# Kernel tuning notes

Hardware: AMD Instinct MI355X
Metric: run time of the kernel (lower is better)

Reference implementation:

```python
import jax, jax.numpy as jnp
import numpy as np

N_USERS = 50000
N_ENTITIES = 100000
D = 64
R = 16
E_UI = 1500000
E_KG = 100000


def setup_inputs() -> dict:
    key = jax.random.key(0)
    ks = jax.random.split(key, 7)
    s = 1.0 / np.sqrt(D)  # ~xavier scale
    return {
        "user_indices": jnp.arange(N_USERS, dtype=jnp.int32),
        "item_indices": jnp.arange(N_ENTITIES, dtype=jnp.int32),
        "edge_index_ui": jax.random.randint(ks[0], (2, E_UI), 0, N_USERS + N_ENTITIES, dtype=jnp.int32),
        "edge_index_kg": jax.random.randint(ks[1], (2, E_KG), 0, N_ENTITIES, dtype=jnp.int32),
        "edge_type_kg": jax.random.randint(ks[2], (E_KG,), 0, R, dtype=jnp.int32),
        "user_table": (jax.random.normal(ks[3], (N_USERS, D)) * s).astype(jnp.float32),
        "entity_table": (jax.random.normal(ks[4], (N_ENTITIES, D)) * s).astype(jnp.float32),
        "W": (jax.random.normal(ks[5], (D, D)) * s).astype(jnp.float32),
        "W_r": (jax.random.normal(ks[6], (R, D, D)) * s).astype(jnp.float32),
    }


def _kgat_layer(x, edge_index, W, W_r, edge_type=None):
    # PyG aggr='add', flow source_to_target: x_j = x[src], x_i = x[dst], scatter to dst
    src, dst = edge_index[0], edge_index[1]
    x_j = x[src]  # [E, D]
    x_i = x[dst]  # [E, D]
    if edge_type is None:
        x_j_t = x_j @ W  # [E, D]
    else:
        # per-edge relation-specific transform: bmm(x_j[:,None,:], W_r[edge_type])
        x_j_t = jnp.einsum('ed,edo->eo', x_j, W_r[edge_type])
    # bi-interaction attention
    x_i_t = x_i @ W
    logits = jnp.sum(x_i_t * x_j_t, axis=1, keepdims=True)  # [E, 1]
    logits = jax.nn.leaky_relu(logits, negative_slope=0.2)
    scores = jax.nn.softmax(logits, axis=0)  # GLOBAL softmax over all edges (as in source)
    msg = scores * x_j_t  # [E, D]
    return jax.ops.segment_sum(msg, dst, num_segments=x.shape[0])


def reference(user_indices, item_indices, edge_index_ui, edge_index_kg, edge_type_kg,
              user_table, entity_table, W, W_r):
    user_embeds = user_table[user_indices]      # [n_users, D]
    item_embeds = entity_table[item_indices]    # [n_entities, D]
    x = jnp.concatenate([user_embeds, item_embeds], axis=0)
    # single layer (layer_dims = [embed_dim])
    x_ui = _kgat_layer(x, edge_index_ui, W, W_r, edge_type=None)
    x_kg = _kgat_layer(item_embeds, edge_index_kg, W, W_r, edge_type=edge_type_kg)
    x = x.at[N_USERS:].add(x_kg)  # faithful to source: overwritten by next line (dead store)
    x = jax.nn.relu(x_ui)
    # F.dropout(training=False) -> identity in eval mode
    return (x[:N_USERS], x[N_USERS:])
```

## Files before the change

kernel.cpp:

```cpp
#include <hip/hip_runtime.h>

#define NU 50000
#define NE 100000
#define NN 150000
#define DD 64
#define EUI 1500000

#define TPB 256
#define NBLK 2048
#define NXB 2344
#define NXH (NXB + NBLK)
#define NBF2 9375
#define NSC 9375

#define XWB_OFF    0ull
#define CNT_OFF    4800000ull
#define SCAL_OFF   4950000ull
#define PSUM_OFF   4950004ull
#define XWQ_OFF    4959424ull

__device__ __forceinline__ unsigned bfpack(float a, float b) {
  unsigned ua = __float_as_uint(a);
  ua = (ua + 0x7fffu + ((ua >> 16) & 1u)) >> 16;
  unsigned ub = __float_as_uint(b);
  ub = (ub + 0x7fffu + ((ub >> 16) & 1u)) & 0xffff0000u;
  return (ua & 0xffffu) | ub;
}

__device__ __forceinline__ unsigned q7pack4(float a, float b, float c, float d) {
  const float m = fmaxf(fmaxf(fabsf(a), fabsf(b)), fmaxf(fabsf(c), fabsf(d)));
  int E = -20;
  if (m >= 3.0517578125e-05f) {
    E = (int)((__float_as_uint(m) >> 23) & 0xffu) - 132;
    E = max(-20, min(-5, E));
  }
  const float s = __uint_as_float((unsigned)(127 - E) << 23);
  const int qa = max(-64, min(63, (int)rintf(a * s)));
  const int qb = max(-64, min(63, (int)rintf(b * s)));
  const int qc = max(-64, min(63, (int)rintf(c * s)));
  const int qd = max(-64, min(63, (int)rintf(d * s)));
  return ((unsigned)(E + 20) << 28) |
         (unsigned)(qa & 0x7f) | ((unsigned)(qb & 0x7f) << 7) |
         ((unsigned)(qc & 0x7f) << 14) | ((unsigned)(qd & 0x7f) << 21);
}

__device__ __forceinline__ void q7unpack4(unsigned v, float& s, float& a,
                                          float& b, float& c, float& d) {
  s = __uint_as_float(((v >> 28) + 107u) << 23);
  a = (float)((int)(v << 25) >> 25);
  b = (float)((int)(v << 18) >> 25);
  c = (float)((int)(v << 11) >> 25);
  d = (float)((int)(v << 4) >> 25);
}

template <int CTRL>
__device__ __forceinline__ float dpp_add(float x) {
  int y = __builtin_amdgcn_update_dpp(0, __float_as_int(x), CTRL, 0xF, 0xF, false);
  return x + __int_as_float(y);
}
__device__ __forceinline__ float row16_sum(float x) {
  x = dpp_add<0x124>(x);
  x = dpp_add<0x128>(x);
  x = dpp_add<0xB1>(x);
  x = dpp_add<0x4E>(x);
  return x;
}

__global__ __launch_bounds__(TPB) void k_xw_hist(const int* __restrict__ uidx,
                                                 const int* __restrict__ iidx,
                                                 const float* __restrict__ ut,
                                                 const float* __restrict__ et,
                                                 const float* __restrict__ W,
                                                 unsigned* __restrict__ xwb,
                                                 unsigned* __restrict__ xwq,
                                                 const int* __restrict__ ei,
                                                 unsigned* __restrict__ cnt,
                                                 int* __restrict__ ssrcp) {
  const int bi = blockIdx.x;
  int idx;
  bool hist;
  if (bi < 2 * NBLK) { hist = (bi & 1); idx = bi >> 1; }
  else               { hist = false;    idx = bi - NBLK; }

  if (hist) {
    for (int e = idx * TPB + threadIdx.x; e < EUI; e += NBLK * TPB) {
      const int dst = ei[EUI + e];
      const int src = ei[e];
      const unsigned r = atomicAdd(&cnt[dst], 1u);
      if (r < 64u) ssrcp[((size_t)dst << 6) + r] = src;
    }
    return;
  }

  __shared__ float Ws[DD * DD];
  __shared__ float Xs[64 * 68];
  const int t = threadIdx.x;
  {
    const float4* W4 = (const float4*)W;
    float4* Ws4 = (float4*)Ws;
#pragma unroll
    for (int i = 0; i < 4; ++i) Ws4[t + i * TPB] = W4[t + i * TPB];
  }
  {
    const int rl = t >> 2, ch = t & 3;
    int row = idx * 64 + rl;
    if (row >= NN) row = NN - 1;
    const float4* s4 = (const float4*)((row < NU)
        ? ut + (size_t)uidx[row] * DD
        : et + (size_t)iidx[row - NU] * DD);
    float4* x4 = (float4*)(Xs + rl * 68);
#pragma unroll
    for (int j = 0; j < 4; ++j) x4[ch + 4 * j] = s4[ch + 4 * j];
  }
  __syncthreads();
  const int q = t & 15, g = t >> 4;
  float4 acc[4] = {{0,0,0,0},{0,0,0,0},{0,0,0,0},{0,0,0,0}};
  const float* __restrict__ wsq = Ws + 4 * q;
  const float* __restrict__ xsg = Xs + (4 * g) * 68;
#pragma unroll 1
  for (int kc = 0; kc < 16; ++kc) {
    const float4 w0 = *(const float4*)(wsq + (4 * kc + 0) * DD);
    const float4 w1 = *(const float4*)(wsq + (4 * kc + 1) * DD);
    const float4 w2 = *(const float4*)(wsq + (4 * kc + 2) * DD);
    const float4 w3 = *(const float4*)(wsq + (4 * kc + 3) * DD);
#pragma unroll
    for (int i = 0; i < 4; ++i) {
      const float4 x = *(const float4*)(xsg + i * 68 + 4 * kc);
      acc[i].x = fmaf(x.x, w0.x, acc[i].x);
      acc[i].y = fmaf(x.x, w0.y, acc[i].y);
      acc[i].z = fmaf(x.x, w0.z, acc[i].z);
      acc[i].w = fmaf(x.x, w0.w, acc[i].w);
      acc[i].x = fmaf(x.y, w1.x, acc[i].x);
      acc[i].y = fmaf(x.y, w1.y, acc[i].y);
      acc[i].z = fmaf(x.y, w1.z, acc[i].z);
      acc[i].w = fmaf(x.y, w1.w, acc[i].w);
      acc[i].x = fmaf(x.z, w2.x, acc[i].x);
      acc[i].y = fmaf(x.z, w2.y, acc[i].y);
      acc[i].z = fmaf(x.z, w2.z, acc[i].z);
      acc[i].w = fmaf(x.z, w2.w, acc[i].w);
      acc[i].x = fmaf(x.w, w3.x, acc[i].x);
      acc[i].y = fmaf(x.w, w3.y, acc[i].y);
      acc[i].z = fmaf(x.w, w3.z, acc[i].z);
      acc[i].w = fmaf(x.w, w3.w, acc[i].w);
    }
  }
#pragma unroll
  for (int i = 0; i < 4; ++i) {
    const int row = idx * 64 + 4 * g + i;
    if (row < NN) {
      uint2 p;
      p.x = bfpack(acc[i].x, acc[i].y);
      p.y = bfpack(acc[i].z, acc[i].w);
      ((uint2*)(xwb + (size_t)row * 32))[q] = p;
      xwq[(size_t)row * 16 + q] = q7pack4(acc[i].x, acc[i].y, acc[i].z, acc[i].w);
    }
  }
}

__global__ __launch_bounds__(TPB) void k_fused(const unsigned* __restrict__ cnt,
                                               const int* ssrcp,
                                               const unsigned* __restrict__ xwb,
                                               const unsigned* __restrict__ xwq,
                                               float* out,
                                               float* __restrict__ psum) {
  const int lane = threadIdx.x & 63;
  const int wv = threadIdx.x >> 6;
  const int sub = lane >> 4;
  const int q = lane & 15;
  const int n = blockIdx.x * 16 + wv * 4 + sub;
  const uint2* __restrict__ x2 = (const uint2*)xwb;
  const uint2 dv = x2[(size_t)n * 16 + q];
  const float vd0 = __uint_as_float(dv.x << 16);
  const float vd1 = __uint_as_float(dv.x & 0xffff0000u);
  const float vd2 = __uint_as_float(dv.y << 16);
  const float vd3 = __uint_as_float(dv.y & 0xffff0000u);
  const int deg = min((int)cnt[n], 64);
  int dmax = deg;
  dmax = max(dmax, __shfl_xor(dmax, 16, 64));
  dmax = max(dmax, __shfl_xor(dmax, 32, 64));
  const size_t base = (size_t)n << 6;
  const int nit = (dmax + 3) >> 2;
  float a0 = 0.f, a1 = 0.f, a2 = 0.f, a3 = 0.f, wacc = 0.f;
  int sl0 = ssrcp[base], sl1 = ssrcp[base + 1];
  int sl2 = ssrcp[base + 2], sl3 = ssrcp[base + 3];
  for (int ii = 0; ii < nit; ++ii) {
    const int it = 4 * ii;
    int s0 = sl0, s1 = sl1, s2 = sl2, s3 = sl3;
    if (ii + 1 < nit) {
      sl0 = ssrcp[base + it + 4];
      sl1 = ssrcp[base + it + 5];
      sl2 = ssrcp[base + it + 6];
      sl3 = ssrcp[base + it + 7];
    }
    const bool act0 = it < deg;
    const bool act1 = it + 1 < deg;
    const bool act2 = it + 2 < deg;
    const bool act3 = it + 3 < deg;
    if (!act0) s0 = 0;
    if (!act1) s1 = 0;
    if (!act2) s2 = 0;
    if (!act3) s3 = 0;
    const unsigned sv0 = xwq[(size_t)s0 * 16 + q];
    const unsigned sv1 = xwq[(size_t)s1 * 16 + q];
    const unsigned sv2 = xwq[(size_t)s2 * 16 + q];
    const unsigned sv3 = xwq[(size_t)s3 * 16 + q];
    float se0, u0, u1, u2, u3;
    float se1, t0, t1, t2, t3;
    float se2, g0, g1, g2, g3;
    float se3, h0, h1, h2, h3;
    q7unpack4(sv0, se0, u0, u1, u2, u3);
    q7unpack4(sv1, se1, t0, t1, t2, t3);
    q7unpack4(sv2, se2, g0, g1, g2, g3);
    q7unpack4(sv3, se3, h0, h1, h2, h3);
    float p0 = vd0 * u0;
    p0 = fmaf(vd1, u1, p0); p0 = fmaf(vd2, u2, p0); p0 = fmaf(vd3, u3, p0);
    float p1 = vd0 * t0;
    p1 = fmaf(vd1, t1, p1); p1 = fmaf(vd2, t2, p1); p1 = fmaf(vd3, t3, p1);
    float p2 = vd0 * g0;
    p2 = fmaf(vd1, g1, p2); p2 = fmaf(vd2, g2, p2); p2 = fmaf(vd3, g3, p2);
    float p3 = vd0 * h0;
    p3 = fmaf(vd1, h1, p3); p3 = fmaf(vd2, h2, p3); p3 = fmaf(vd3, h3, p3);
    p0 *= se0;
    p1 *= se1;
    p2 *= se2;
    p3 *= se3;
    p0 = row16_sum(p0);
    p1 = row16_sum(p1);
    p2 = row16_sum(p2);
    p3 = row16_sum(p3);
    const float l0 = (p0 > 0.f) ? p0 : 0.2f * p0;
    const float l1 = (p1 > 0.f) ? p1 : 0.2f * p1;
    const float l2 = (p2 > 0.f) ? p2 : 0.2f * p2;
    const float l3 = (p3 > 0.f) ? p3 : 0.2f * p3;
    float w0 = __expf(l0);
    float w1 = __expf(l1);
    float w2 = __expf(l2);
    float w3 = __expf(l3);
    if (!act0) w0 = 0.f;
    if (!act1) w1 = 0.f;
    if (!act2) w2 = 0.f;
    if (!act3) w3 = 0.f;
    const float ws0 = w0 * se0;
    const float ws1 = w1 * se1;
    const float ws2 = w2 * se2;
    const float ws3 = w3 * se3;
    a0 = fmaf(ws0, u0, a0); a1 = fmaf(ws0, u1, a1);
    a2 = fmaf(ws0, u2, a2); a3 = fmaf(ws0, u3, a3);
    a0 = fmaf(ws1, t0, a0); a1 = fmaf(ws1, t1, a1);
    a2 = fmaf(ws1, t2, a2); a3 = fmaf(ws1, t3, a3);
    a0 = fmaf(ws2, g0, a0); a1 = fmaf(ws2, g1, a1);
    a2 = fmaf(ws2, g2, a2); a3 = fmaf(ws2, g3, a3);
    a0 = fmaf(ws3, h0, a0); a1 = fmaf(ws3, h1, a1);
    a2 = fmaf(ws3, h2, a2); a3 = fmaf(ws3, h3, a3);
    wacc += (w0 + w1) + (w2 + w3);
  }
  float4 r = {a0, a1, a2, a3};
  ((float4*)(out + (size_t)n * DD))[q] = r;
  __shared__ float sm[16];
  if (q == 0) sm[wv * 4 + sub] = wacc;
  __syncthreads();
  if (threadIdx.x == 0) {
    float s = 0.f;
#pragma unroll
    for (int i = 0; i < 16; ++i) s += sm[i];
    psum[blockIdx.x] = s;
  }
}

__global__ __launch_bounds__(TPB) void k_rsum(const float* __restrict__ psum,
                                              float* __restrict__ scal) {
  float s = 0.f;
  for (int i = threadIdx.x; i < NBF2; i += TPB) s += psum[i];
#pragma unroll
  for (int off = 32; off; off >>= 1) s += __shfl_xor(s, off, 64);
  __shared__ float sm[4];
  if ((threadIdx.x & 63) == 0) sm[threadIdx.x >> 6] = s;
  __syncthreads();
  if (threadIdx.x == 0) scal[0] = sm[0] + sm[1] + sm[2] + sm[3];
}

__global__ __launch_bounds__(TPB) void k_scale(float* __restrict__ out,
                                               const float* __restrict__ scal) {
  const float inv = 1.0f / scal[0];
  const int i = blockIdx.x * TPB + threadIdx.x;
  float4* o4 = (float4*)out;
  float4 v = o4[i];
  v.x = fmaxf(v.x * inv, 0.f);
  v.y = fmaxf(v.y * inv, 0.f);
  v.z = fmaxf(v.z * inv, 0.f);
  v.w = fmaxf(v.w * inv, 0.f);
  o4[i] = v;
}

extern "C" void kernel_launch(void* const* d_in, const int* in_sizes, int n_in,
                              void* d_out, int out_size, void* d_ws, size_t ws_size,
                              hipStream_t stream) {
  const int* uidx = (const int*)d_in[0];
  const int* iidx = (const int*)d_in[1];
  const int* ei_ui = (const int*)d_in[2];
  const float* ut = (const float*)d_in[5];
  const float* et = (const float*)d_in[6];
  const float* W = (const float*)d_in[7];

  float* out = (float*)d_out;
  float* ws = (float*)d_ws;
  unsigned* xwb = (unsigned*)(ws + XWB_OFF);
  unsigned* cnt = (unsigned*)(ws + CNT_OFF);
  float* scal = ws + SCAL_OFF;
  float* psum = ws + PSUM_OFF;
  unsigned* xwq = (unsigned*)(ws + XWQ_OFF);
  int* ssrcp = (int*)d_out;

  (void)hipMemsetAsync(cnt, 0, (size_t)NN * sizeof(unsigned), stream);

  k_xw_hist<<<NXH, TPB, 0, stream>>>(uidx, iidx, ut, et, W, xwb, xwq, ei_ui,
                                     cnt, ssrcp);
  k_fused<<<NBF2, TPB, 0, stream>>>(cnt, ssrcp, xwb, xwq, out, psum);
  k_rsum<<<1, TPB, 0, stream>>>(psum, scal);
  k_scale<<<NSC, TPB, 0, stream>>>(out, scal);
}
```

Measured before the change: 263.1 us.

## Split histogram by destination range to overlap second half with gather of first

The edge histogram/bucketing is split into two destination ranges. The first half runs alongside the XW transform, and the second half runs in the same launch as the aggregation of the first half of nodes. The remaining nodes are aggregated in a third kernel. This aims to hide the atomic bucketing cost behind compute, but each histogram pass now reads the full edge list twice, adding extra dst reads and divergent skips. The neighbor-index prefetch also becomes a single int4 load.

```diff
diff --git a/kernel.cpp b/kernel.cpp
--- a/kernel.cpp
+++ b/kernel.cpp
@@ -5,11 +5,15 @@
 #define NN 150000
 #define DD 64
 #define EUI 1500000
+#define SPLIT 75008
 
 #define TPB 256
 #define NBLK 2048
 #define NXB 2344
 #define NXH (NXB + NBLK)
+#define NBFA 4688
+#define NBFB 4687
+#define NHF (NBFA + NBLK)
 #define NBF2 9375
 #define NSC 9375
 
@@ -66,108 +70,31 @@
   return x;
 }
 
-__global__ __launch_bounds__(TPB) void k_xw_hist(const int* __restrict__ uidx,
-                                                 const int* __restrict__ iidx,
-                                                 const float* __restrict__ ut,
-                                                 const float* __restrict__ et,
-                                                 const float* __restrict__ W,
-                                                 unsigned* __restrict__ xwb,
-                                                 unsigned* __restrict__ xwq,
-                                                 const int* __restrict__ ei,
-                                                 unsigned* __restrict__ cnt,
-                                                 int* __restrict__ ssrcp) {
-  const int bi = blockIdx.x;
-  int idx;
-  bool hist;
-  if (bi < 2 * NBLK) { hist = (bi & 1); idx = bi >> 1; }
-  else               { hist = false;    idx = bi - NBLK; }
-
-  if (hist) {
-    for (int e = idx * TPB + threadIdx.x; e < EUI; e += NBLK * TPB) {
-      const int dst = ei[EUI + e];
-      const int src = ei[e];
-      const unsigned r = atomicAdd(&cnt[dst], 1u);
-      if (r < 64u) ssrcp[((size_t)dst << 6) + r] = src;
-    }
-    return;
-  }
-
-  __shared__ float Ws[DD * DD];
-  __shared__ float Xs[64 * 68];
-  const int t = threadIdx.x;
-  {
-    const float4* W4 = (const float4*)W;
-    float4* Ws4 = (float4*)Ws;
-#pragma unroll
-    for (int i = 0; i < 4; ++i) Ws4[t + i * TPB] = W4[t + i * TPB];
-  }
-  {
-    const int rl = t >> 2, ch = t & 3;
-    int row = idx * 64 + rl;
-    if (row >= NN) row = NN - 1;
-    const float4* s4 = (const float4*)((row < NU)
-        ? ut + (size_t)uidx[row] * DD
-        : et + (size_t)iidx[row - NU] * DD);
-    float4* x4 = (float4*)(Xs + rl * 68);
-#pragma unroll
-    for (int j = 0; j < 4; ++j) x4[ch + 4 * j] = s4[ch + 4 * j];
-  }
-  __syncthreads();
-  const int q = t & 15, g = t >> 4;
-  float4 acc[4] = {{0,0,0,0},{0,0,0,0},{0,0,0,0},{0,0,0,0}};
-  const float* __restrict__ wsq = Ws + 4 * q;
-  const float* __restrict__ xsg = Xs + (4 * g) * 68;
-#pragma unroll 1
-  for (int kc = 0; kc < 16; ++kc) {
-    const float4 w0 = *(const float4*)(wsq + (4 * kc + 0) * DD);
-    const float4 w1 = *(const float4*)(wsq + (4 * kc + 1) * DD);
-    const float4 w2 = *(const float4*)(wsq + (4 * kc + 2) * DD);
-    const float4 w3 = *(const float4*)(wsq + (4 * kc + 3) * DD);
-#pragma unroll
-    for (int i = 0; i < 4; ++i) {
-      const float4 x = *(const float4*)(xsg + i * 68 + 4 * kc);
-      acc[i].x = fmaf(x.x, w0.x, acc[i].x);
-      acc[i].y = fmaf(x.x, w0.y, acc[i].y);
-      acc[i].z = fmaf(x.x, w0.z, acc[i].z);
-      acc[i].w = fmaf(x.x, w0.w, acc[i].w);
-      acc[i].x = fmaf(x.y, w1.x, acc[i].x);
-      acc[i].y = fmaf(x.y, w1.y, acc[i].y);
-      acc[i].z = fmaf(x.y, w1.z, acc[i].z);
-      acc[i].w = fmaf(x.y, w1.w, acc[i].w);
-      acc[i].x = fmaf(x.z, w2.x, acc[i].x);
-      acc[i].y = fmaf(x.z, w2.y, acc[i].y);
-      acc[i].z = fmaf(x.z, w2.z, acc[i].z);
-      acc[i].w = fmaf(x.z, w2.w, acc[i].w);
-      acc[i].x = fmaf(x.w, w3.x, acc[i].x);
-      acc[i].y = fmaf(x.w, w3.y, acc[i].y);
-      acc[i].z = fmaf(x.w, w3.z, acc[i].z);
-      acc[i].w = fmaf(x.w, w3.w, acc[i].w);
-    }
-  }
-#pragma unroll
-  for (int i = 0; i < 4; ++i) {
-    const int row = idx * 64 + 4 * g + i;
-    if (row < NN) {
-      uint2 p;
-      p.x = bfpack(acc[i].x, acc[i].y);
-      p.y = bfpack(acc[i].z, acc[i].w);
-      ((uint2*)(xwb + (size_t)row * 32))[q] = p;
-      xwq[(size_t)row * 16 + q] = q7pack4(acc[i].x, acc[i].y, acc[i].z, acc[i].w);
-    }
-  }
-}
-
-__global__ __launch_bounds__(TPB) void k_fused(const unsigned* __restrict__ cnt,
-                                               const int* ssrcp,
-                                               const unsigned* __restrict__ xwb,
-                                               const unsigned* __restrict__ xwq,
-                                               float* out,
-                                               float* __restrict__ psum) {
+__device__ __forceinline__ void hist_body(int idx, const int* __restrict__ ei,
+                                          unsigned* __restrict__ cnt,
+                                          int* __restrict__ ssrcp,
+                                          int lo, int hi) {
+  for (int e = idx * TPB + threadIdx.x; e < EUI; e += NBLK * TPB) {
+    const int dst = ei[EUI + e];
+    if (dst < lo || dst >= hi) continue;
+    const int src = ei[e];
+    const unsigned r = atomicAdd(&cnt[dst], 1u);
+    if (r < 64u) ssrcp[((size_t)dst << 6) + r] = src;
+  }
+}
+
+__device__ __forceinline__ void fused_tile(int tile,
+                                           const unsigned* __restrict__ cnt,
+                                           const int* ssrcp,
+                                           const unsigned* __restrict__ xwb,
+                                           const unsigned* __restrict__ xwq,
+                                           float* out,
+                                           float* __restrict__ psum) {
   const int lane = threadIdx.x & 63;
   const int wv = threadIdx.x >> 6;
   const int sub = lane >> 4;
   const int q = lane & 15;
-  const int n = blockIdx.x * 16 + wv * 4 + sub;
+  const int n = tile * 16 + wv * 4 + sub;
   const uint2* __restrict__ x2 = (const uint2*)xwb;
   const uint2 dv = x2[(size_t)n * 16 + q];
   const float vd0 = __uint_as_float(dv.x << 16);
@@ -181,17 +108,11 @@
   const size_t base = (size_t)n << 6;
   const int nit = (dmax + 3) >> 2;
   float a0 = 0.f, a1 = 0.f, a2 = 0.f, a3 = 0.f, wacc = 0.f;
-  int sl0 = ssrcp[base], sl1 = ssrcp[base + 1];
-  int sl2 = ssrcp[base + 2], sl3 = ssrcp[base + 3];
+  int4 sl = *(const int4*)(ssrcp + base);
   for (int ii = 0; ii < nit; ++ii) {
     const int it = 4 * ii;
-    int s0 = sl0, s1 = sl1, s2 = sl2, s3 = sl3;
-    if (ii + 1 < nit) {
-      sl0 = ssrcp[base + it + 4];
-      sl1 = ssrcp[base + it + 5];
-      sl2 = ssrcp[base + it + 6];
-      sl3 = ssrcp[base + it + 7];
-    }
+    int s0 = sl.x, s1 = sl.y, s2 = sl.z, s3 = sl.w;
+    if (ii + 1 < nit) sl = *(const int4*)(ssrcp + base + it + 4);
     const bool act0 = it < deg;
     const bool act1 = it + 1 < deg;
     const bool act2 = it + 2 < deg;
@@ -263,8 +184,123 @@
     float s = 0.f;
 #pragma unroll
     for (int i = 0; i < 16; ++i) s += sm[i];
-    psum[blockIdx.x] = s;
-  }
+    psum[tile] = s;
+  }
+}
+
+__global__ __launch_bounds__(TPB) void k_xw_histA(const int* __restrict__ uidx,
+                                                  const int* __restrict__ iidx,
+                                                  const float* __restrict__ ut,
+                                                  const float* __restrict__ et,
+                                                  const float* __restrict__ W,
+                                                  unsigned* __restrict__ xwb,
+                                                  unsigned* __restrict__ xwq,
+                                                  const int* __restrict__ ei,
+                                                  unsigned* __restrict__ cnt,
+                                                  int* __restrict__ ssrcp) {
+  const int bi = blockIdx.x;
+  int idx;
+  bool hist;
+  if (bi < 2 * NBLK) { hist = (bi & 1); idx = bi >> 1; }
+  else               { hist = false;    idx = bi - NBLK; }
+
+  if (hist) {
+    hist_body(idx, ei, cnt, ssrcp, 0, SPLIT);
+    return;
+  }
+
+  __shared__ float Ws[DD * DD];
+  __shared__ float Xs[64 * 68];
+  const int t = threadIdx.x;
+  {
+    const float4* W4 = (const float4*)W;
+    float4* Ws4 = (float4*)Ws;
+#pragma unroll
+    for (int i = 0; i < 4; ++i) Ws4[t + i * TPB] = W4[t + i * TPB];
+  }
+  {
+    const int rl = t >> 2, ch = t & 3;
+    int row = idx * 64 + rl;
+    if (row >= NN) row = NN - 1;
+    const float4* s4 = (const float4*)((row < NU)
+        ? ut + (size_t)uidx[row] * DD
+        : et + (size_t)iidx[row - NU] * DD);
+    float4* x4 = (float4*)(Xs + rl * 68);
+#pragma unroll
+    for (int j = 0; j < 4; ++j) x4[ch + 4 * j] = s4[ch + 4 * j];
+  }
+  __syncthreads();
+  const int q = t & 15, g = t >> 4;
+  float4 acc[4] = {{0,0,0,0},{0,0,0,0},{0,0,0,0},{0,0,0,0}};
+  const float* __restrict__ wsq = Ws + 4 * q;
+  const float* __restrict__ xsg = Xs + (4 * g) * 68;
+#pragma unroll 1
+  for (int kc = 0; kc < 16; ++kc) {
+    const float4 w0 = *(const float4*)(wsq + (4 * kc + 0) * DD);
+    const float4 w1 = *(const float4*)(wsq + (4 * kc + 1) * DD);
+    const float4 w2 = *(const float4*)(wsq + (4 * kc + 2) * DD);
+    const float4 w3 = *(const float4*)(wsq + (4 * kc + 3) * DD);
+#pragma unroll
+    for (int i = 0; i < 4; ++i) {
+      const float4 x = *(const float4*)(xsg + i * 68 + 4 * kc);
+      acc[i].x = fmaf(x.x, w0.x, acc[i].x);
+      acc[i].y = fmaf(x.x, w0.y, acc[i].y);
+      acc[i].z = fmaf(x.x, w0.z, acc[i].z);
+      acc[i].w = fmaf(x.x, w0.w, acc[i].w);
+      acc[i].x = fmaf(x.y, w1.x, acc[i].x);
+      acc[i].y = fmaf(x.y, w1.y, acc[i].y);
+      acc[i].z = fmaf(x.y, w1.z, acc[i].z);
+      acc[i].w = fmaf(x.y, w1.w, acc[i].w);
+      acc[i].x = fmaf(x.z, w2.x, acc[i].x);
+      acc[i].y = fmaf(x.z, w2.y, acc[i].y);
+      acc[i].z = fmaf(x.z, w2.z, acc[i].z);
+      acc[i].w = fmaf(x.z, w2.w, acc[i].w);
+      acc[i].x = fmaf(x.w, w3.x, acc[i].x);
+      acc[i].y = fmaf(x.w, w3.y, acc[i].y);
+      acc[i].z = fmaf(x.w, w3.z, acc[i].z);
+      acc[i].w = fmaf(x.w, w3.w, acc[i].w);
+    }
+  }
+#pragma unroll
+  for (int i = 0; i < 4; ++i) {
+    const int row = idx * 64 + 4 * g + i;
+    if (row < NN) {
+      uint2 p;
+      p.x = bfpack(acc[i].x, acc[i].y);
+      p.y = bfpack(acc[i].z, acc[i].w);
+      ((uint2*)(xwb + (size_t)row * 32))[q] = p;
+      xwq[(size_t)row * 16 + q] = q7pack4(acc[i].x, acc[i].y, acc[i].z, acc[i].w);
+    }
+  }
+}
+
+__global__ __launch_bounds__(TPB) void k_histB_fusedA(const int* __restrict__ ei,
+                                                      unsigned* __restrict__ cnt,
+                                                      int* ssrcp,
+                                                      const unsigned* __restrict__ xwb,
+                                                      const unsigned* __restrict__ xwq,
+                                                      float* out,
+                                                      float* __restrict__ psum) {
+  const int bi = blockIdx.x;
+  int idx;
+  bool hist;
+  if (bi < 2 * NBLK) { hist = (bi & 1); idx = bi >> 1; }
+  else               { hist = false;    idx = bi - NBLK; }
+
+  if (hist) {
+    hist_body(idx, ei, cnt, ssrcp, SPLIT, NN);
+    return;
+  }
+  fused_tile(idx, cnt, ssrcp, xwb, xwq, out, psum);
+}
+
+__global__ __launch_bounds__(TPB) void k_fusedB(const unsigned* __restrict__ cnt,
+                                                const int* ssrcp,
+                                                const unsigned* __restrict__ xwb,
+                                                const unsigned* __restrict__ xwq,
+                                                float* out,
+                                                float* __restrict__ psum) {
+  fused_tile(NBFA + blockIdx.x, cnt, ssrcp, xwb, xwq, out, psum);
 }
 
 __global__ __launch_bounds__(TPB) void k_rsum(const float* __restrict__ psum,
@@ -313,9 +349,10 @@
 
   (void)hipMemsetAsync(cnt, 0, (size_t)NN * sizeof(unsigned), stream);
 
-  k_xw_hist<<<NXH, TPB, 0, stream>>>(uidx, iidx, ut, et, W, xwb, xwq, ei_ui,
-                                     cnt, ssrcp);
-  k_fused<<<NBF2, TPB, 0, stream>>>(cnt, ssrcp, xwb, xwq, out, psum);
+  k_xw_histA<<<NXH, TPB, 0, stream>>>(uidx, iidx, ut, et, W, xwb, xwq, ei_ui,
+                                      cnt, ssrcp);
+  k_histB_fusedA<<<NHF, TPB, 0, stream>>>(ei_ui, cnt, ssrcp, xwb, xwq, out, psum);
+  k_fusedB<<<NBFB, TPB, 0, stream>>>(cnt, ssrcp, xwb, xwq, out, psum);
   k_rsum<<<1, TPB, 0, stream>>>(psum, scal);
   k_scale<<<NSC, TPB, 0, stream>>>(out, scal);
 }
```

Result: faster. 246.3 us (-6.4%).
